# Performance work log

Measured on AMD Instinct MI355X. Metric: run time of the kernel, lower is better.

Reference implementation:

```python
import jax, jax.numpy as jnp
import numpy as np

N_NODES = 100000
N_EDGES = 1600000
IN_CH = 64
HID = 64
OUT_CH = 16


def setup_inputs() -> dict:
    key = jax.random.key(0)
    ks = jax.random.split(key, 8)
    x = jax.random.normal(ks[0], (N_NODES, IN_CH), dtype=jnp.float32)
    edge_index = jax.random.randint(ks[1], (2, N_EDGES), 0, N_NODES, dtype=jnp.int64)
    s = 1.0 / np.sqrt(IN_CH)
    W1l = jax.random.normal(ks[2], (HID, IN_CH), dtype=jnp.float32) * s
    W1r = jax.random.normal(ks[3], (HID, IN_CH), dtype=jnp.float32) * s
    b1 = jnp.zeros((HID,), dtype=jnp.float32)
    W2l = jax.random.normal(ks[4], (HID, HID), dtype=jnp.float32) * s
    W2r = jax.random.normal(ks[5], (HID, HID), dtype=jnp.float32) * s
    b2 = jnp.zeros((HID,), dtype=jnp.float32)
    Wlin = jax.random.normal(ks[6], (OUT_CH, HID), dtype=jnp.float32) * s
    blin = jnp.zeros((OUT_CH,), dtype=jnp.float32)
    return {"x": x, "edge_index": edge_index, "W1l": W1l, "b1": b1, "W1r": W1r,
            "W2l": W2l, "b2": b2, "W2r": W2r, "Wlin": Wlin, "blin": blin}


def _sage_conv(x, src, dst, Wl, b, Wr):
    # PyG SAGEConv with mean aggregation:
    # out = lin_l(mean_{j in N(i)} x_j) + lin_r(x_i); bias lives in lin_l.
    msgs = x[src]                                              # [E, F] gather
    summed = jax.ops.segment_sum(msgs, dst, num_segments=N_NODES)  # [N, F]
    cnt = jax.ops.segment_sum(jnp.ones((src.shape[0],), x.dtype), dst,
                              num_segments=N_NODES)            # [N]
    agg = summed / jnp.maximum(cnt, 1.0)[:, None]              # mean, deg-0 safe
    return agg @ Wl.T + b + x @ Wr.T


def reference(x, edge_index, W1l, b1, W1r, W2l, b2, W2r, Wlin, blin):
    src, dst = edge_index[0], edge_index[1]
    h = jax.nn.relu(_sage_conv(x, src, dst, W1l, b1, W1r))
    h = jax.nn.relu(_sage_conv(h, src, dst, W2l, b2, W2r))
    return h @ Wlin.T + blin
```

## Files before the change

### kernel.cpp

```cpp
#include <hip/hip_runtime.h>

#define NN 100000
#define NE 1600000

#define BSHIFT 9
#define BWIDTH 512
#define NBUCK 196
#define SLOTS 12288
#define CHUNK 4096
#define B1_BLOCKS ((NE + CHUNK - 1) / CHUNK)
#define GEMM_BLOCKS ((NN + 63) / 64)
#define AGG_CAP 1024

typedef float    v2f __attribute__((ext_vector_type(2)));
typedef unsigned v2u __attribute__((ext_vector_type(2)));
typedef short    bf16x8 __attribute__((ext_vector_type(8)));
typedef float    f32x4  __attribute__((ext_vector_type(4)));

__device__ __forceinline__ float u2f(unsigned u) {
    union { unsigned u; float f; } v; v.u = u; return v.f;
}
__device__ __forceinline__ unsigned f2u(float f) {
    union { float f; unsigned u; } v; v.f = f; return v.u;
}
__device__ __forceinline__ unsigned f2bf(float f) {
    unsigned u = f2u(f);
    return (u + 0x7FFFu + ((u >> 16) & 1u)) >> 16;
}
__device__ __forceinline__ v2f unpk(unsigned x) {
    v2u w; w[0] = x << 16; w[1] = x & 0xFFFF0000u;
    union { v2u u; v2f f; } c; c.u = w; return c.f;
}
__device__ __forceinline__ int wave_incl_scan(int v, int lane) {
    #pragma unroll
    for (int off = 1; off < 64; off <<= 1) {
        int u = __shfl_up(v, off);
        if (lane >= off) v += u;
    }
    return v;
}

__global__ void detect_mode_kernel(const int* ei32, int* flag, int* bcnt) {
    __shared__ int any_nonzero;
    if (threadIdx.x == 0) any_nonzero = 0;
    if (threadIdx.x < NBUCK) bcnt[threadIdx.x] = 0;
    __syncthreads();
    int idx = 1 + 2 * threadIdx.x;
    if (ei32[idx] != 0) atomicOr(&any_nonzero, 1);
    __syncthreads();
    if (threadIdx.x == 0) flag[0] = (any_nonzero == 0) ? 1 : 0;
}

__device__ __forceinline__ void load_edge(const void* ei, int is64, int e,
                                          int& s, int& d) {
    if (is64) {
        const long long* p = (const long long*)ei;
        s = (int)p[e];
        d = (int)p[NE + e];
    } else {
        const int* p = (const int*)ei;
        s = p[e];
        d = p[NE + e];
    }
}

template<int BF16IN>
__device__ __forceinline__ void gemm_mfma_body(
    char* smem, const void* __restrict__ featv,
    const float* __restrict__ Wl, const float* __restrict__ Wr,
    const float* __restrict__ bias,
    unsigned* __restrict__ outt, unsigned* __restrict__ outr,
    int tile, int t)
{
    unsigned short* Als = (unsigned short*)smem;
    unsigned short* Bls = (unsigned short*)(smem + 9216);
    const int lane = t & 63, w = t >> 6;
    const int m0 = tile * 64;
    const float*    featf = (const float*)featv;
    const unsigned* featu = (const unsigned*)featv;

    #pragma unroll
    for (int rep = 0; rep < 2; ++rep) {
        int task = t + 256 * rep;
        int row = task >> 3, s = task & 7;
        int gn = m0 + row;
        uint4 u;
        if (BF16IN) {
            u = (gn < NN) ? *(const uint4*)(featu + (size_t)gn * 32 + 4 * s)
                          : make_uint4(0u, 0u, 0u, 0u);
        } else {
            if (gn < NN) {
                float4 v0 = *(const float4*)(featf + (size_t)gn * 64 + 8 * s);
                float4 v1 = *(const float4*)(featf + (size_t)gn * 64 + 8 * s + 4);
                u.x = f2bf(v0.x) | (f2bf(v0.y) << 16);
                u.y = f2bf(v0.z) | (f2bf(v0.w) << 16);
                u.z = f2bf(v1.x) | (f2bf(v1.y) << 16);
                u.w = f2bf(v1.z) | (f2bf(v1.w) << 16);
            } else u = make_uint4(0u, 0u, 0u, 0u);
        }
        *(uint4*)(Als + row * 72 + 8 * s) = u;
    }
    #pragma unroll
    for (int rep = 0; rep < 4; ++rep) {
        int task = t + 256 * rep;
        int c = task >> 3, s = task & 7;
        const float* Wsrc = (c < 64) ? (Wl + (size_t)c * 64)
                                     : (Wr + (size_t)(c - 64) * 64);
        float4 v0 = *(const float4*)(Wsrc + 8 * s);
        float4 v1 = *(const float4*)(Wsrc + 8 * s + 4);
        uint4 u;
        u.x = f2bf(v0.x) | (f2bf(v0.y) << 16);
        u.y = f2bf(v0.z) | (f2bf(v0.w) << 16);
        u.z = f2bf(v1.x) | (f2bf(v1.y) << 16);
        u.w = f2bf(v1.z) | (f2bf(v1.w) << 16);
        *(uint4*)(Bls + c * 72 + 8 * s) = u;
    }
    __syncthreads();

    const int r = lane & 15, g = lane >> 4;
    const int cw0 = 32 * w;

    bf16x8 bf[2][2];
    #pragma unroll
    for (int ct = 0; ct < 2; ++ct)
        #pragma unroll
        for (int ks = 0; ks < 2; ++ks) {
            int c = cw0 + 16 * ct + r;
            bf[ct][ks] = *(const bf16x8*)(Bls + c * 72 + (ks * 4 + g) * 8);
        }

    f32x4 acc[4][2];
    #pragma unroll
    for (int nt = 0; nt < 4; ++nt)
        #pragma unroll
        for (int ct = 0; ct < 2; ++ct)
            acc[nt][ct] = (f32x4){0.f, 0.f, 0.f, 0.f};

    #pragma unroll
    for (int nt = 0; nt < 4; ++nt) {
        bf16x8 af[2];
        #pragma unroll
        for (int ks = 0; ks < 2; ++ks) {
            int rr = nt * 16 + r;
            af[ks] = *(const bf16x8*)(Als + rr * 72 + (ks * 4 + g) * 8);
        }
        #pragma unroll
        for (int ct = 0; ct < 2; ++ct)
            #pragma unroll
            for (int ks = 0; ks < 2; ++ks)
                acc[nt][ct] = __builtin_amdgcn_mfma_f32_16x16x32_bf16(
                    af[ks], bf[ct][ks], acc[nt][ct], 0, 0, 0);
    }

    unsigned short* Tb = (unsigned short*)outt;
    unsigned short* Rb = (unsigned short*)outr;
    #pragma unroll
    for (int ct = 0; ct < 2; ++ct) {
        int c = cw0 + 16 * ct + r;
        float badd = (c >= 64) ? bias[c - 64] : 0.f;
        unsigned short* dst = (c < 64) ? (Tb + c) : (Rb + (c - 64));
        #pragma unroll
        for (int nt = 0; nt < 4; ++nt)
            #pragma unroll
            for (int i = 0; i < 4; ++i) {
                int row = m0 + nt * 16 + g * 4 + i;
                if (row < NN)
                    dst[(size_t)row * 64] = (unsigned short)f2bf(acc[nt][ct][i] + badd);
            }
    }
}

__global__ __launch_bounds__(256) void b1_gemm1_kernel(
    const void* ei, const int* flag,
    int* __restrict__ bcnt, int* __restrict__ bpk,
    const float* __restrict__ x,
    const float* __restrict__ W1l, const float* __restrict__ W1r,
    const float* __restrict__ b1,
    unsigned* __restrict__ T, unsigned* __restrict__ R)
{
    __shared__ __align__(16) char smem[27648];
    const int t = threadIdx.x;

    if (blockIdx.x >= B1_BLOCKS) {
        if (blockIdx.x == B1_BLOCKS && t < 32) T[(size_t)NN * 32 + t] = 0u;
        gemm_mfma_body<0>(smem, x, W1l, W1r, b1, T, R, blockIdx.x - B1_BLOCKS, t);
        return;
    }

    int* stage = (int*)smem;
    unsigned char* sbuck = (unsigned char*)(smem + 16384);
    int* hist  = (int*)(smem + 20480);
    int* scanb = (int*)(smem + 21264);
    int* gbase = (int*)(smem + 22048);
    int* lofs  = (int*)(smem + 22832);
    int* wsum  = (int*)(smem + 23616);

    const int is64 = *flag;
    const int e0 = blockIdx.x * CHUNK;
    const int nE = min(CHUNK, NE - e0);
    const int lane = t & 63, wvi = t >> 6;

    for (int i = t; i < NBUCK; i += 256) { hist[i] = 0; lofs[i] = 0; }
    __syncthreads();

    int sr[16], dr[16];
    #pragma unroll
    for (int rr = 0; rr < 16; ++rr) {
        int e = e0 + t + 256 * rr;
        if (e < NE) load_edge(ei, is64, e, sr[rr], dr[rr]);
        else dr[rr] = -1;
    }
    #pragma unroll
    for (int rr = 0; rr < 16; ++rr)
        if (dr[rr] >= 0) atomicAdd(&hist[dr[rr] >> BSHIFT], 1);
    __syncthreads();

    int v = (t < NBUCK) ? hist[t] : 0;
    int s = wave_incl_scan(v, lane);
    if (lane == 63) wsum[wvi] = s;
    __syncthreads();
    int add = 0;
    #pragma unroll
    for (int k = 0; k < 3; ++k) if (wvi > k) add += wsum[k];
    s += add;
    if (t < NBUCK) {
        scanb[t] = s - v;
        gbase[t] = atomicAdd(&bcnt[t], v);
    }
    __syncthreads();

    #pragma unroll
    for (int rr = 0; rr < 16; ++rr) {
        if (dr[rr] >= 0) {
            int b = dr[rr] >> BSHIFT;
            int p = scanb[b] + atomicAdd(&lofs[b], 1);
            stage[p] = (sr[rr] << BSHIFT) | (dr[rr] & (BWIDTH - 1));
            sbuck[p] = (unsigned char)b;
        }
    }
    __syncthreads();

    for (int i = t; i < nE; i += 256) {
        int b = sbuck[i];
        int off = gbase[b] + (i - scanb[b]);
        if (off < SLOTS) bpk[(size_t)b * SLOTS + off] = stage[i];
    }
}

__global__ __launch_bounds__(512) void bucket_to_csr_kernel(
    const int* __restrict__ bcnt, const int* __restrict__ bpk,
    int* __restrict__ rowptr, int* __restrict__ colb)
{
    __shared__ int ldeg[512], lptr[512], lcnt[512], sc[512], wsum[8];
    const int t = threadIdx.x, b = blockIdx.x;
    const int lane = t & 63, wvi = t >> 6;

    int v = (t < NBUCK) ? bcnt[t] : 0;
    int s = wave_incl_scan(v, lane);
    if (lane == 63) wsum[wvi] = s;
    __syncthreads();
    int add = 0;
    #pragma unroll
    for (int k = 0; k < 7; ++k) if (wvi > k) add += wsum[k];
    s += add;
    sc[t] = s;
    __syncthreads();
    const int base = (b == 0) ? 0 : sc[b - 1];
    if (b == 0 && t == 0) rowptr[NN] = NE;
    __syncthreads();

    ldeg[t] = 0; lcnt[t] = 0;
    __syncthreads();

    const int n0 = b << BSHIFT;
    const int cnt = min(bcnt[b], SLOTS);
    const int* src = bpk + (size_t)b * SLOTS;
    for (int i = t; i < cnt; i += 512)
        atomicAdd(&ldeg[src[i] & (BWIDTH - 1)], 1);
    __syncthreads();

    int a = ldeg[t];
    int s2 = wave_incl_scan(a, lane);
    if (lane == 63) wsum[wvi] = s2;
    __syncthreads();
    int add2 = 0;
    #pragma unroll
    for (int k = 0; k < 7; ++k) if (wvi > k) add2 += wsum[k];
    s2 += add2;
    lptr[t] = s2 - a;
    __syncthreads();

    int gn = n0 + t;
    if (gn < NN) rowptr[gn] = base + lptr[t];

    for (int i = t; i < cnt; i += 512) {
        int p = src[i];
        int li = p & (BWIDTH - 1);
        int pos = lptr[li] + atomicAdd(&lcnt[li], 1);
        colb[base + pos] = (p >> BSHIFT) << 7;
    }
}

__global__ __launch_bounds__(256) void gemm2_kernel(
    const unsigned* __restrict__ feat,
    const float* __restrict__ Wl, const float* __restrict__ Wr,
    const float* __restrict__ bias,
    unsigned* __restrict__ outt, unsigned* __restrict__ outr)
{
    __shared__ __align__(16) char smem[27648];
    gemm_mfma_body<1>(smem, feat, Wl, Wr, bias, outt, outr, blockIdx.x, threadIdx.x);
}

#define AGG_STEP(O0, O1, O2, O3)                                              \
    {                                                                         \
        int o0 = O0, o1 = O1, o2 = O2, o3 = O3;                               \
        o0 = (jj      < end) ? o0 : zoff;                                     \
        o1 = (jj + 4  < end) ? o1 : zoff;                                     \
        o2 = (jj + 8  < end) ? o2 : zoff;                                     \
        o3 = (jj + 12 < end) ? o3 : zoff;                                     \
        uint4 u0 = *(const uint4*)(tb + (size_t)(unsigned)o0 + 16 * c8);      \
        uint4 u1 = *(const uint4*)(tb + (size_t)(unsigned)o1 + 16 * c8);      \
        uint4 u2 = *(const uint4*)(tb + (size_t)(unsigned)o2 + 16 * c8);      \
        uint4 u3 = *(const uint4*)(tb + (size_t)(unsigned)o3 + 16 * c8);      \
        a0 += unpk(u0.x); a1 += unpk(u0.y); a2 += unpk(u0.z); a3 += unpk(u0.w);\
        b0 += unpk(u1.x); b1 += unpk(u1.y); b2 += unpk(u1.z); b3 += unpk(u1.w);\
        a0 += unpk(u2.x); a1 += unpk(u2.y); a2 += unpk(u2.z); a3 += unpk(u2.w);\
        b0 += unpk(u3.x); b1 += unpk(u3.y); b2 += unpk(u3.z); b3 += unpk(u3.w);\
    }

__global__ void aggregate_relu_kernel(const int* __restrict__ rowptr,
                                      const int* __restrict__ colb,
                                      const unsigned* __restrict__ tt,
                                      unsigned* rh) {
    __shared__ int lcol[AGG_CAP];
    const int t = threadIdx.x;
    const int n0 = blockIdx.x * 8;
    const int lane = t & 63;
    const int w = t >> 6;
    const int half = lane >> 5;
    const int slot = (lane >> 3) & 3;
    const int c8   = lane & 7;
    const int node = n0 + 2 * w + half;

    const int cbeg  = rowptr[n0];
    const int cendB = rowptr[min(n0 + 8, NN)];
    const int total = cendB - cbeg;
    const bool fast = (total <= AGG_CAP);
    if (fast) {
        for (int i = t; i < total; i += 256) lcol[i] = colb[cbeg + i];
    }
    __syncthreads();

    if (node >= NN) return;
    const int beg = rowptr[node], end = rowptr[node + 1];
    const int deg = end - beg;
    int niter = (deg + 3) >> 2;
    niter = max(niter, __shfl_xor(niter, 32));

    const char* tb = (const char*)tt;
    const int zoff = NN * 128;
    v2f a0 = {0.f, 0.f}, a1 = {0.f, 0.f}, a2 = {0.f, 0.f}, a3 = {0.f, 0.f};
    v2f b0 = {0.f, 0.f}, b1 = {0.f, 0.f}, b2 = {0.f, 0.f}, b3 = {0.f, 0.f};

    int jj = beg + slot;
    int it = 0;
    if (fast) {
        for (; it + 4 <= niter; it += 4, jj += 16) {
            int jc0 = min(jj,      end - 1) - cbeg;
            int jc1 = min(jj + 4,  end - 1) - cbeg;
            int jc2 = min(jj + 8,  end - 1) - cbeg;
            int jc3 = min(jj + 12, end - 1) - cbeg;
            AGG_STEP(lcol[jc0], lcol[jc1], lcol[jc2], lcol[jc3])
        }
        for (; it < niter; ++it, jj += 4) {
            int jc0 = min(jj, end - 1) - cbeg;
            int o0 = lcol[jc0];
            o0 = (jj < end) ? o0 : zoff;
            uint4 u0 = *(const uint4*)(tb + (size_t)(unsigned)o0 + 16 * c8);
            a0 += unpk(u0.x); a1 += unpk(u0.y); a2 += unpk(u0.z); a3 += unpk(u0.w);
        }
    } else {
        for (; it + 4 <= niter; it += 4, jj += 16) {
            int jc0 = min(jj,      end - 1);
            int jc1 = min(jj + 4,  end - 1);
            int jc2 = min(jj + 8,  end - 1);
            int jc3 = min(jj + 12, end - 1);
            AGG_STEP(colb[jc0], colb[jc1], colb[jc2], colb[jc3])
        }
        for (; it < niter; ++it, jj += 4) {
            int jc0 = min(jj, end - 1);
            int o0 = colb[jc0];
            o0 = (jj < end) ? o0 : zoff;
            uint4 u0 = *(const uint4*)(tb + (size_t)(unsigned)o0 + 16 * c8);
            a0 += unpk(u0.x); a1 += unpk(u0.y); a2 += unpk(u0.z); a3 += unpk(u0.w);
        }
    }
    a0 += b0; a1 += b1; a2 += b2; a3 += b3;

    a0[0] += __shfl_xor(a0[0], 8);  a0[1] += __shfl_xor(a0[1], 8);
    a1[0] += __shfl_xor(a1[0], 8);  a1[1] += __shfl_xor(a1[1], 8);
    a2[0] += __shfl_xor(a2[0], 8);  a2[1] += __shfl_xor(a2[1], 8);
    a3[0] += __shfl_xor(a3[0], 8);  a3[1] += __shfl_xor(a3[1], 8);
    a0[0] += __shfl_xor(a0[0], 16); a0[1] += __shfl_xor(a0[1], 16);
    a1[0] += __shfl_xor(a1[0], 16); a1[1] += __shfl_xor(a1[1], 16);
    a2[0] += __shfl_xor(a2[0], 16); a2[1] += __shfl_xor(a2[1], 16);
    a3[0] += __shfl_xor(a3[0], 16); a3[1] += __shfl_xor(a3[1], 16);

    if (slot == 0) {
        float inv = 1.0f / fmaxf((float)deg, 1.0f);
        unsigned* p = rh + (size_t)node * 32 + 4 * c8;
        uint4 rr = *(const uint4*)p;
        v2f q0 = unpk(rr.x), q1 = unpk(rr.y), q2 = unpk(rr.z), q3 = unpk(rr.w);
        float h0 = fmaxf(fmaf(a0[0], inv, q0[0]), 0.0f);
        float h1 = fmaxf(fmaf(a0[1], inv, q0[1]), 0.0f);
        float h2 = fmaxf(fmaf(a1[0], inv, q1[0]), 0.0f);
        float h3 = fmaxf(fmaf(a1[1], inv, q1[1]), 0.0f);
        float h4 = fmaxf(fmaf(a2[0], inv, q2[0]), 0.0f);
        float h5 = fmaxf(fmaf(a2[1], inv, q2[1]), 0.0f);
        float h6 = fmaxf(fmaf(a3[0], inv, q3[0]), 0.0f);
        float h7 = fmaxf(fmaf(a3[1], inv, q3[1]), 0.0f);
        uint4 wv4;
        wv4.x = f2bf(h0) | (f2bf(h1) << 16);
        wv4.y = f2bf(h2) | (f2bf(h3) << 16);
        wv4.z = f2bf(h4) | (f2bf(h5) << 16);
        wv4.w = f2bf(h6) | (f2bf(h7) << 16);
        *(uint4*)p = wv4;
    }
}

__global__ __launch_bounds__(256) void head_kernel(
    const unsigned* __restrict__ hu,
    const float* __restrict__ Wlin,
    const float* __restrict__ blin,
    float* __restrict__ out)
{
    __shared__ float As[64][132];
    __shared__ float Bs[64][18];
    const int t = threadIdx.x;

    {
        int c = t & 15, j = t >> 4;
        float4 v = *(const float4*)(Wlin + (size_t)c * 64 + 4 * j);
        Bs[4 * j + 0][c] = v.x; Bs[4 * j + 1][c] = v.y;
        Bs[4 * j + 2][c] = v.z; Bs[4 * j + 3][c] = v.w;
    }
    const int m0 = blockIdx.x * 128;
    {
        int kq = t & 7;
        int nb = t >> 3;
        for (int rep = 0; rep < 4; ++rep) {
            int n = nb + 32 * rep;
            int gn = m0 + n;
            uint4 u = (gn < NN) ? *(const uint4*)(hu + (size_t)gn * 32 + 4 * kq)
                                : make_uint4(0u, 0u, 0u, 0u);
            int kk = 8 * kq;
            As[kk + 0][n] = u2f(u.x << 16); As[kk + 1][n] = u2f(u.x & 0xFFFF0000u);
            As[kk + 2][n] = u2f(u.y << 16); As[kk + 3][n] = u2f(u.y & 0xFFFF0000u);
            As[kk + 4][n] = u2f(u.z << 16); As[kk + 5][n] = u2f(u.z & 0xFFFF0000u);
            As[kk + 6][n] = u2f(u.w << 16); As[kk + 7][n] = u2f(u.w & 0xFFFF0000u);
        }
    }
    __syncthreads();

    const int tn = t & 31;
    const int tc = t >> 5;
    const int c0 = 2 * tc;
    float acc[4][2];
    #pragma unroll
    for (int i = 0; i < 4; ++i) { acc[i][0] = blin[c0]; acc[i][1] = blin[c0 + 1]; }

    #pragma unroll 16
    for (int k = 0; k < 64; ++k) {
        float4 a = *(const float4*)&As[k][4 * tn];
        float b0 = Bs[k][c0], b1 = Bs[k][c0 + 1];
        float av[4] = {a.x, a.y, a.z, a.w};
        #pragma unroll
        for (int i = 0; i < 4; ++i) {
            acc[i][0] = fmaf(av[i], b0, acc[i][0]);
            acc[i][1] = fmaf(av[i], b1, acc[i][1]);
        }
    }
    #pragma unroll
    for (int i = 0; i < 4; ++i) {
        int gn = m0 + 4 * tn + i;
        if (gn < NN)
            *(float2*)(out + (size_t)gn * 16 + c0) = make_float2(acc[i][0], acc[i][1]);
    }
}

extern "C" void kernel_launch(void* const* d_in, const int* in_sizes, int n_in,
                              void* d_out, int out_size, void* d_ws, size_t ws_size,
                              hipStream_t stream) {
    const float* x    = (const float*)d_in[0];
    const void*  ei   = d_in[1];
    const float* W1l  = (const float*)d_in[2];
    const float* b1   = (const float*)d_in[3];
    const float* W1r  = (const float*)d_in[4];
    const float* W2l  = (const float*)d_in[5];
    const float* b2   = (const float*)d_in[6];
    const float* W2r  = (const float*)d_in[7];
    const float* Wlin = (const float*)d_in[8];
    const float* blin = (const float*)d_in[9];
    float* out = (float*)d_out;

    char* w = (char*)d_ws;
    int*      flag   = (int*)w;
    int*      bcnt   = (int*)(w + (size_t)4 * 1024);
    int*      rowptr = (int*)(w + (size_t)1024 * 1024);
    int*      colb   = (int*)(w + (size_t)2 * 1024 * 1024);
    int*      bpk    = (int*)(w + (size_t)10 * 1024 * 1024);
    unsigned* T      = (unsigned*)(w + (size_t)30 * 1024 * 1024);
    unsigned* R      = (unsigned*)(w + (size_t)43 * 1024 * 1024);

    detect_mode_kernel<<<1, 256, 0, stream>>>((const int*)ei, flag, bcnt);

    b1_gemm1_kernel<<<B1_BLOCKS + GEMM_BLOCKS, 256, 0, stream>>>(
        ei, flag, bcnt, bpk, x, W1l, W1r, b1, T, R);

    bucket_to_csr_kernel<<<NBUCK, 512, 0, stream>>>(bcnt, bpk, rowptr, colb);

    const int aggBlocks = (NN + 7) / 8;
    const int headBlocks = (NN + 127) / 128;

    aggregate_relu_kernel<<<aggBlocks, 256, 0, stream>>>(rowptr, colb, T, R);

    gemm2_kernel<<<GEMM_BLOCKS, 256, 0, stream>>>(R, W2l, W2r, b2, T, R);
    aggregate_relu_kernel<<<aggBlocks, 256, 0, stream>>>(rowptr, colb, T, R);

    head_kernel<<<headBlocks, 256, 0, stream>>>(R, Wlin, blin, out);
}
```

Baseline: 144.5 us.

## Split transformed features into four column-quarter planes for gather locality

The GEMM output T is now stored as four separate planes of 16 bf16 columns (32 bytes per row) instead of 64-column rows. The aggregation kernel walks the planes one after another, with 16 edge slots and 2 lanes per edge in each pass, and column offsets are rescaled to match. The goal is to shrink each gathered row's footprint to 32 bytes so a plane fits better in cache, which may raise the hit rate on random neighbor gathers. In exchange, every edge index is read four times, the GEMM stores are narrower and more scattered, and each edge costs four 16-byte loads, possibly hurting coalescing.

```diff
diff --git a/kernel.cpp b/kernel.cpp
--- a/kernel.cpp
+++ b/kernel.cpp
@@ -154,19 +154,36 @@
 
     unsigned short* Tb = (unsigned short*)outt;
     unsigned short* Rb = (unsigned short*)outr;
-    #pragma unroll
-    for (int ct = 0; ct < 2; ++ct) {
-        int c = cw0 + 16 * ct + r;
-        float badd = (c >= 64) ? bias[c - 64] : 0.f;
-        unsigned short* dst = (c < 64) ? (Tb + c) : (Rb + (c - 64));
-        #pragma unroll
-        for (int nt = 0; nt < 4; ++nt)
+    if (cw0 < 64) {
+        #pragma unroll
+        for (int ct = 0; ct < 2; ++ct) {
+            int c = cw0 + 16 * ct + r;
+            int q = c >> 4;
+            unsigned short* dst = Tb + (size_t)q * (NN + 1) * 16 + (c & 15);
             #pragma unroll
-            for (int i = 0; i < 4; ++i) {
-                int row = m0 + nt * 16 + g * 4 + i;
-                if (row < NN)
-                    dst[(size_t)row * 64] = (unsigned short)f2bf(acc[nt][ct][i] + badd);
-            }
+            for (int nt = 0; nt < 4; ++nt)
+                #pragma unroll
+                for (int i = 0; i < 4; ++i) {
+                    int row = m0 + nt * 16 + g * 4 + i;
+                    if (row < NN)
+                        dst[(size_t)row * 16] = (unsigned short)f2bf(acc[nt][ct][i]);
+                }
+        }
+    } else {
+        #pragma unroll
+        for (int ct = 0; ct < 2; ++ct) {
+            int c = cw0 + 16 * ct + r;
+            float badd = bias[c - 64];
+            unsigned short* dst = Rb + (c - 64);
+            #pragma unroll
+            for (int nt = 0; nt < 4; ++nt)
+                #pragma unroll
+                for (int i = 0; i < 4; ++i) {
+                    int row = m0 + nt * 16 + g * 4 + i;
+                    if (row < NN)
+                        dst[(size_t)row * 64] = (unsigned short)f2bf(acc[nt][ct][i] + badd);
+                }
+        }
     }
 }
 
@@ -182,7 +199,10 @@
     const int t = threadIdx.x;
 
     if (blockIdx.x >= B1_BLOCKS) {
-        if (blockIdx.x == B1_BLOCKS && t < 32) T[(size_t)NN * 32 + t] = 0u;
+        if (blockIdx.x == B1_BLOCKS && t < 32) {
+            int q = t >> 3, i = t & 7;
+            T[(size_t)q * (NN + 1) * 8 + (size_t)NN * 8 + i] = 0u;
+        }
         gemm_mfma_body<0>(smem, x, W1l, W1r, b1, T, R, blockIdx.x - B1_BLOCKS, t);
         return;
     }
@@ -297,7 +317,7 @@
         int p = src[i];
         int li = p & (BWIDTH - 1);
         int pos = lptr[li] + atomicAdd(&lcnt[li], 1);
-        colb[base + pos] = (p >> BSHIFT) << 7;
+        colb[base + pos] = (p >> BSHIFT) << 5;
     }
 }
 
@@ -310,23 +330,6 @@
     __shared__ __align__(16) char smem[27648];
     gemm_mfma_body<1>(smem, feat, Wl, Wr, bias, outt, outr, blockIdx.x, threadIdx.x);
 }
-
-#define AGG_STEP(O0, O1, O2, O3)                                              \
-    {                                                                         \
-        int o0 = O0, o1 = O1, o2 = O2, o3 = O3;                               \
-        o0 = (jj      < end) ? o0 : zoff;                                     \
-        o1 = (jj + 4  < end) ? o1 : zoff;                                     \
-        o2 = (jj + 8  < end) ? o2 : zoff;                                     \
-        o3 = (jj + 12 < end) ? o3 : zoff;                                     \
-        uint4 u0 = *(const uint4*)(tb + (size_t)(unsigned)o0 + 16 * c8);      \
-        uint4 u1 = *(const uint4*)(tb + (size_t)(unsigned)o1 + 16 * c8);      \
-        uint4 u2 = *(const uint4*)(tb + (size_t)(unsigned)o2 + 16 * c8);      \
-        uint4 u3 = *(const uint4*)(tb + (size_t)(unsigned)o3 + 16 * c8);      \
-        a0 += unpk(u0.x); a1 += unpk(u0.y); a2 += unpk(u0.z); a3 += unpk(u0.w);\
-        b0 += unpk(u1.x); b1 += unpk(u1.y); b2 += unpk(u1.z); b3 += unpk(u1.w);\
-        a0 += unpk(u2.x); a1 += unpk(u2.y); a2 += unpk(u2.z); a3 += unpk(u2.w);\
-        b0 += unpk(u3.x); b1 += unpk(u3.y); b2 += unpk(u3.z); b3 += unpk(u3.w);\
-    }
 
 __global__ void aggregate_relu_kernel(const int* __restrict__ rowptr,
                                       const int* __restrict__ colb,
@@ -338,8 +341,8 @@
     const int lane = t & 63;
     const int w = t >> 6;
     const int half = lane >> 5;
-    const int slot = (lane >> 3) & 3;
-    const int c8   = lane & 7;
+    const int slot = (lane >> 1) & 15;
+    const int cq   = lane & 1;
     const int node = n0 + 2 * w + half;
 
     const int cbeg  = rowptr[n0];
@@ -354,77 +357,52 @@
     if (node >= NN) return;
     const int beg = rowptr[node], end = rowptr[node + 1];
     const int deg = end - beg;
-    int niter = (deg + 3) >> 2;
+    int niter = (deg + 15) >> 4;
     niter = max(niter, __shfl_xor(niter, 32));
 
     const char* tb = (const char*)tt;
-    const int zoff = NN * 128;
-    v2f a0 = {0.f, 0.f}, a1 = {0.f, 0.f}, a2 = {0.f, 0.f}, a3 = {0.f, 0.f};
-    v2f b0 = {0.f, 0.f}, b1 = {0.f, 0.f}, b2 = {0.f, 0.f}, b3 = {0.f, 0.f};
-
-    int jj = beg + slot;
-    int it = 0;
-    if (fast) {
-        for (; it + 4 <= niter; it += 4, jj += 16) {
-            int jc0 = min(jj,      end - 1) - cbeg;
-            int jc1 = min(jj + 4,  end - 1) - cbeg;
-            int jc2 = min(jj + 8,  end - 1) - cbeg;
-            int jc3 = min(jj + 12, end - 1) - cbeg;
-            AGG_STEP(lcol[jc0], lcol[jc1], lcol[jc2], lcol[jc3])
-        }
-        for (; it < niter; ++it, jj += 4) {
-            int jc0 = min(jj, end - 1) - cbeg;
-            int o0 = lcol[jc0];
-            o0 = (jj < end) ? o0 : zoff;
-            uint4 u0 = *(const uint4*)(tb + (size_t)(unsigned)o0 + 16 * c8);
-            a0 += unpk(u0.x); a1 += unpk(u0.y); a2 += unpk(u0.z); a3 += unpk(u0.w);
-        }
-    } else {
-        for (; it + 4 <= niter; it += 4, jj += 16) {
-            int jc0 = min(jj,      end - 1);
-            int jc1 = min(jj + 4,  end - 1);
-            int jc2 = min(jj + 8,  end - 1);
-            int jc3 = min(jj + 12, end - 1);
-            AGG_STEP(colb[jc0], colb[jc1], colb[jc2], colb[jc3])
-        }
-        for (; it < niter; ++it, jj += 4) {
-            int jc0 = min(jj, end - 1);
-            int o0 = colb[jc0];
-            o0 = (jj < end) ? o0 : zoff;
-            uint4 u0 = *(const uint4*)(tb + (size_t)(unsigned)o0 + 16 * c8);
-            a0 += unpk(u0.x); a1 += unpk(u0.y); a2 += unpk(u0.z); a3 += unpk(u0.w);
-        }
-    }
-    a0 += b0; a1 += b1; a2 += b2; a3 += b3;
-
-    a0[0] += __shfl_xor(a0[0], 8);  a0[1] += __shfl_xor(a0[1], 8);
-    a1[0] += __shfl_xor(a1[0], 8);  a1[1] += __shfl_xor(a1[1], 8);
-    a2[0] += __shfl_xor(a2[0], 8);  a2[1] += __shfl_xor(a2[1], 8);
-    a3[0] += __shfl_xor(a3[0], 8);  a3[1] += __shfl_xor(a3[1], 8);
-    a0[0] += __shfl_xor(a0[0], 16); a0[1] += __shfl_xor(a0[1], 16);
-    a1[0] += __shfl_xor(a1[0], 16); a1[1] += __shfl_xor(a1[1], 16);
-    a2[0] += __shfl_xor(a2[0], 16); a2[1] += __shfl_xor(a2[1], 16);
-    a3[0] += __shfl_xor(a3[0], 16); a3[1] += __shfl_xor(a3[1], 16);
-
-    if (slot == 0) {
-        float inv = 1.0f / fmaxf((float)deg, 1.0f);
-        unsigned* p = rh + (size_t)node * 32 + 4 * c8;
-        uint4 rr = *(const uint4*)p;
-        v2f q0 = unpk(rr.x), q1 = unpk(rr.y), q2 = unpk(rr.z), q3 = unpk(rr.w);
-        float h0 = fmaxf(fmaf(a0[0], inv, q0[0]), 0.0f);
-        float h1 = fmaxf(fmaf(a0[1], inv, q0[1]), 0.0f);
-        float h2 = fmaxf(fmaf(a1[0], inv, q1[0]), 0.0f);
-        float h3 = fmaxf(fmaf(a1[1], inv, q1[1]), 0.0f);
-        float h4 = fmaxf(fmaf(a2[0], inv, q2[0]), 0.0f);
-        float h5 = fmaxf(fmaf(a2[1], inv, q2[1]), 0.0f);
-        float h6 = fmaxf(fmaf(a3[0], inv, q3[0]), 0.0f);
-        float h7 = fmaxf(fmaf(a3[1], inv, q3[1]), 0.0f);
-        uint4 wv4;
-        wv4.x = f2bf(h0) | (f2bf(h1) << 16);
-        wv4.y = f2bf(h2) | (f2bf(h3) << 16);
-        wv4.z = f2bf(h4) | (f2bf(h5) << 16);
-        wv4.w = f2bf(h6) | (f2bf(h7) << 16);
-        *(uint4*)p = wv4;
+    const int zoff = NN * 32;
+    const float inv = 1.0f / fmaxf((float)deg, 1.0f);
+
+    #pragma unroll
+    for (int q = 0; q < 4; ++q) {
+        const size_t qbase = (size_t)q * (NN + 1) * 32;
+        v2f a0 = {0.f, 0.f}, a1 = {0.f, 0.f}, a2 = {0.f, 0.f}, a3 = {0.f, 0.f};
+        int jj = beg + slot;
+        for (int it = 0; it < niter; ++it, jj += 16) {
+            int o;
+            if (fast) { int jc = min(jj, end - 1) - cbeg; o = lcol[jc]; }
+            else      { int jc = min(jj, end - 1);        o = colb[jc]; }
+            o = (jj < end) ? o : zoff;
+            uint4 u = *(const uint4*)(tb + qbase + (size_t)(unsigned)o + 16 * cq);
+            a0 += unpk(u.x); a1 += unpk(u.y); a2 += unpk(u.z); a3 += unpk(u.w);
+        }
+        #pragma unroll
+        for (int m = 2; m <= 16; m <<= 1) {
+            a0[0] += __shfl_xor(a0[0], m); a0[1] += __shfl_xor(a0[1], m);
+            a1[0] += __shfl_xor(a1[0], m); a1[1] += __shfl_xor(a1[1], m);
+            a2[0] += __shfl_xor(a2[0], m); a2[1] += __shfl_xor(a2[1], m);
+            a3[0] += __shfl_xor(a3[0], m); a3[1] += __shfl_xor(a3[1], m);
+        }
+        if (slot == 0) {
+            unsigned* p = rh + (size_t)node * 32 + q * 8 + cq * 4;
+            uint4 rr = *(const uint4*)p;
+            v2f q0 = unpk(rr.x), q1 = unpk(rr.y), q2 = unpk(rr.z), q3 = unpk(rr.w);
+            float h0 = fmaxf(fmaf(a0[0], inv, q0[0]), 0.0f);
+            float h1 = fmaxf(fmaf(a0[1], inv, q0[1]), 0.0f);
+            float h2 = fmaxf(fmaf(a1[0], inv, q1[0]), 0.0f);
+            float h3 = fmaxf(fmaf(a1[1], inv, q1[1]), 0.0f);
+            float h4 = fmaxf(fmaf(a2[0], inv, q2[0]), 0.0f);
+            float h5 = fmaxf(fmaf(a2[1], inv, q2[1]), 0.0f);
+            float h6 = fmaxf(fmaf(a3[0], inv, q3[0]), 0.0f);
+            float h7 = fmaxf(fmaf(a3[1], inv, q3[1]), 0.0f);
+            uint4 wv4;
+            wv4.x = f2bf(h0) | (f2bf(h1) << 16);
+            wv4.y = f2bf(h2) | (f2bf(h3) << 16);
+            wv4.z = f2bf(h4) | (f2bf(h5) << 16);
+            wv4.w = f2bf(h6) | (f2bf(h7) << 16);
+            *(uint4*)p = wv4;
+        }
     }
 }
 
```

New measurement: 252.7 us. +74.8%, slower.

## Fuse output linear head into final aggregation kernel

Applied to the files above, without the earlier changes.

Templates the aggregate kernel with a FINAL flag so that, in the second layer, the bf16 hidden rows go into shared memory instead of global memory. A 16-output linear layer with bias is then applied in the same block, and the separate head kernel is dropped. This removes one kernel launch and the global write and re-read of the final hidden layer. In exchange, every block loads Wlin into shared memory, uses more shared memory and adds an extra barrier. The early return for out-of-range nodes is also removed, which is only safe because the node count divides evenly by 8.

```diff
diff --git a/kernel.cpp b/kernel.cpp
--- a/kernel.cpp
+++ b/kernel.cpp
@@ -328,11 +328,17 @@
         b0 += unpk(u3.x); b1 += unpk(u3.y); b2 += unpk(u3.z); b3 += unpk(u3.w);\
     }
 
+template<int FINAL>
 __global__ void aggregate_relu_kernel(const int* __restrict__ rowptr,
                                       const int* __restrict__ colb,
                                       const unsigned* __restrict__ tt,
-                                      unsigned* rh) {
+                                      unsigned* rh,
+                                      const float* __restrict__ Wlin,
+                                      const float* __restrict__ blin,
+                                      float* __restrict__ out) {
     __shared__ int lcol[AGG_CAP];
+    __shared__ float wls[1024];
+    __shared__ unsigned short hbuf[8][72];
     const int t = threadIdx.x;
     const int n0 = blockIdx.x * 8;
     const int lane = t & 63;
@@ -349,9 +355,11 @@
     if (fast) {
         for (int i = t; i < total; i += 256) lcol[i] = colb[cbeg + i];
     }
-    __syncthreads();
-
-    if (node >= NN) return;
+    if (FINAL) {
+        for (int i = t; i < 1024; i += 256) wls[i] = Wlin[i];
+    }
+    __syncthreads();
+
     const int beg = rowptr[node], end = rowptr[node + 1];
     const int deg = end - beg;
     int niter = (deg + 3) >> 2;
@@ -424,67 +432,29 @@
         wv4.y = f2bf(h2) | (f2bf(h3) << 16);
         wv4.z = f2bf(h4) | (f2bf(h5) << 16);
         wv4.w = f2bf(h6) | (f2bf(h7) << 16);
-        *(uint4*)p = wv4;
-    }
-}
-
-__global__ __launch_bounds__(256) void head_kernel(
-    const unsigned* __restrict__ hu,
-    const float* __restrict__ Wlin,
-    const float* __restrict__ blin,
-    float* __restrict__ out)
-{
-    __shared__ float As[64][132];
-    __shared__ float Bs[64][18];
-    const int t = threadIdx.x;
-
-    {
-        int c = t & 15, j = t >> 4;
-        float4 v = *(const float4*)(Wlin + (size_t)c * 64 + 4 * j);
-        Bs[4 * j + 0][c] = v.x; Bs[4 * j + 1][c] = v.y;
-        Bs[4 * j + 2][c] = v.z; Bs[4 * j + 3][c] = v.w;
-    }
-    const int m0 = blockIdx.x * 128;
-    {
-        int kq = t & 7;
-        int nb = t >> 3;
-        for (int rep = 0; rep < 4; ++rep) {
-            int n = nb + 32 * rep;
-            int gn = m0 + n;
-            uint4 u = (gn < NN) ? *(const uint4*)(hu + (size_t)gn * 32 + 4 * kq)
-                                : make_uint4(0u, 0u, 0u, 0u);
-            int kk = 8 * kq;
-            As[kk + 0][n] = u2f(u.x << 16); As[kk + 1][n] = u2f(u.x & 0xFFFF0000u);
-            As[kk + 2][n] = u2f(u.y << 16); As[kk + 3][n] = u2f(u.y & 0xFFFF0000u);
-            As[kk + 4][n] = u2f(u.z << 16); As[kk + 5][n] = u2f(u.z & 0xFFFF0000u);
-            As[kk + 6][n] = u2f(u.w << 16); As[kk + 7][n] = u2f(u.w & 0xFFFF0000u);
-        }
-    }
-    __syncthreads();
-
-    const int tn = t & 31;
-    const int tc = t >> 5;
-    const int c0 = 2 * tc;
-    float acc[4][2];
-    #pragma unroll
-    for (int i = 0; i < 4; ++i) { acc[i][0] = blin[c0]; acc[i][1] = blin[c0 + 1]; }
-
-    #pragma unroll 16
-    for (int k = 0; k < 64; ++k) {
-        float4 a = *(const float4*)&As[k][4 * tn];
-        float b0 = Bs[k][c0], b1 = Bs[k][c0 + 1];
-        float av[4] = {a.x, a.y, a.z, a.w};
-        #pragma unroll
-        for (int i = 0; i < 4; ++i) {
-            acc[i][0] = fmaf(av[i], b0, acc[i][0]);
-            acc[i][1] = fmaf(av[i], b1, acc[i][1]);
-        }
-    }
-    #pragma unroll
-    for (int i = 0; i < 4; ++i) {
-        int gn = m0 + 4 * tn + i;
-        if (gn < NN)
-            *(float2*)(out + (size_t)gn * 16 + c0) = make_float2(acc[i][0], acc[i][1]);
+        if (FINAL) {
+            *(uint4*)&hbuf[2 * w + half][8 * c8] = wv4;
+        } else {
+            *(uint4*)p = wv4;
+        }
+    }
+
+    if (FINAL) {
+        __syncthreads();
+        if (t < 128) {
+            int i = t >> 4, cc = t & 15;
+            int gnode = n0 + i;
+            const unsigned* hrow = (const unsigned*)hbuf[i];
+            float acc = blin[cc];
+            #pragma unroll
+            for (int k2 = 0; k2 < 32; ++k2) {
+                v2f hv = unpk(hrow[k2]);
+                acc = fmaf(hv[0], wls[cc * 64 + 2 * k2], acc);
+                acc = fmaf(hv[1], wls[cc * 64 + 2 * k2 + 1], acc);
+            }
+            if (gnode < NN)
+                out[(size_t)gnode * 16 + cc] = acc;
+        }
     }
 }
 
@@ -520,12 +490,12 @@
     bucket_to_csr_kernel<<<NBUCK, 512, 0, stream>>>(bcnt, bpk, rowptr, colb);
 
     const int aggBlocks = (NN + 7) / 8;
-    const int headBlocks = (NN + 127) / 128;
-
-    aggregate_relu_kernel<<<aggBlocks, 256, 0, stream>>>(rowptr, colb, T, R);
+
+    aggregate_relu_kernel<0><<<aggBlocks, 256, 0, stream>>>(
+        rowptr, colb, T, R, nullptr, nullptr, nullptr);
 
     gemm2_kernel<<<GEMM_BLOCKS, 256, 0, stream>>>(R, W2l, W2r, b2, T, R);
-    aggregate_relu_kernel<<<aggBlocks, 256, 0, stream>>>(rowptr, colb, T, R);
-
-    head_kernel<<<headBlocks, 256, 0, stream>>>(R, Wlin, blin, out);
-}
+
+    aggregate_relu_kernel<1><<<aggBlocks, 256, 0, stream>>>(
+        rowptr, colb, T, R, Wlin, blin, out);
+}
```

Measured after the change: 168.5 us. +16.5%, slower.
